# Performance work log

Measured on AMD Instinct MI355X. Metric: run time of the kernel, lower is better.

## Reference

```python
import jax, jax.numpy as jnp
import numpy as np

S, H, P, NL, PL = 128, 1024, 1024, 2, 32  # string_size, hidden, program_size, layers, program_length
T_IN, T_OUT = 64, 64


def _run_lstm(xs, h0, c0, layers):
    """Multi-layer LSTM over sequence xs [T, in]. PyTorch gate order i,f,g,o.
    h0, c0: [NL, H]. Returns (top-layer outputs [T, H], hT [NL,H], cT [NL,H])."""
    hs, cs = [], []
    for l, (Wih, Whh, bih, bhh) in enumerate(layers):
        b = bih + bhh
        def step(carry, x, Wih=Wih, Whh=Whh, b=b):
            h, c = carry
            g = Wih @ x + Whh @ h + b           # [4H]
            i, f, gg, o = jnp.split(g, 4)
            c = jax.nn.sigmoid(f) * c + jax.nn.sigmoid(i) * jnp.tanh(gg)
            h = jax.nn.sigmoid(o) * jnp.tanh(c)
            return (h, c), h
        (hT, cT), xs = jax.lax.scan(step, (h0[l], c0[l]), xs)
        hs.append(hT); cs.append(cT)
    return xs, jnp.stack(hs), jnp.stack(cs)


def setup_inputs() -> dict:
    key = jax.random.key(0)
    keys = iter(jax.random.split(key, 64))
    bound = 1.0 / np.sqrt(H)
    def u(shape):
        return jax.random.uniform(next(keys), shape, minval=-bound, maxval=bound, dtype=jnp.float32)
    d = {}
    for pre, in0 in (("in", S), ("out", S), ("pr", H)):
        for l in range(NL):
            isz = in0 if l == 0 else H
            d[f"{pre}_Wih{l}"] = u((4 * H, isz))
            d[f"{pre}_Whh{l}"] = u((4 * H, H))
            d[f"{pre}_bih{l}"] = u((4 * H,))
            d[f"{pre}_bhh{l}"] = u((4 * H,))
    d["lin_W"] = u((P, H))
    d["lin_b"] = u((P,))
    d["input_seq"] = jax.random.randint(next(keys), (T_IN,), 0, S)
    d["output_seq"] = jax.random.randint(next(keys), (T_OUT,), 0, S)
    return d


def reference(in_Wih0, in_Whh0, in_bih0, in_bhh0, in_Wih1, in_Whh1, in_bih1, in_bhh1,
              out_Wih0, out_Whh0, out_bih0, out_bhh0, out_Wih1, out_Whh1, out_bih1, out_bhh1,
              pr_Wih0, pr_Whh0, pr_bih0, pr_bhh0, pr_Wih1, pr_Whh1, pr_bih1, pr_bhh1,
              lin_W, lin_b, input_seq, output_seq):
    in_layers = [(in_Wih0, in_Whh0, in_bih0, in_bhh0), (in_Wih1, in_Whh1, in_bih1, in_bhh1)]
    out_layers = [(out_Wih0, out_Whh0, out_bih0, out_bhh0), (out_Wih1, out_Whh1, out_bih1, out_bhh1)]
    pr_layers = [(pr_Wih0, pr_Whh0, pr_bih0, pr_bhh0), (pr_Wih1, pr_Whh1, pr_bih1, pr_bhh1)]

    x_in = jax.nn.one_hot(input_seq, S, dtype=jnp.float32)    # [T_IN, S]
    x_out = jax.nn.one_hot(output_seq, S, dtype=jnp.float32)  # [T_OUT, S]

    h = jnp.zeros((NL, H), dtype=jnp.float32)
    c = jnp.zeros((NL, H), dtype=jnp.float32)
    _, h, c = _run_lstm(x_in, h, c, in_layers)
    _, h, c = _run_lstm(x_out, h, c, out_layers)

    # Faithful to source: previous_hidden is set once and never updated inside the loop,
    # so the program LSTM sees the SAME input vector at every decode step.
    prev_h = h[-1]                                            # [H]
    xs = jnp.broadcast_to(prev_h, (PL, H))
    ys, h, c = _run_lstm(xs, h, c, pr_layers)                 # [PL, H]
    return ys @ lin_W.T + lin_b                                # [PL, P]
```

## Files before the change

kernel.cpp:

```cpp
#include <hip/hip_runtime.h>
#include <hip/hip_fp16.h>
#include <cmath>

#define HDIM 1024
#define TPB 512
#define NWG 256
#define M4 4194304ull
#define WS_WOFF 65536ull
#define CVT_TOTAL 42991616ull
#define WS_NEEDED (WS_WOFF + CVT_TOTAL * 2ull)

typedef unsigned long long ulong64;
typedef unsigned int uint32;
typedef _Float16 h2f __attribute__((ext_vector_type(2)));

__device__ __forceinline__ ulong64 ld_g8(const ulong64* p) {
  return __hip_atomic_load(p, __ATOMIC_RELAXED, __HIP_MEMORY_SCOPE_AGENT);
}
__device__ __forceinline__ void st_gu(uint32* p, uint32 v) {
  __hip_atomic_store(p, v, __ATOMIC_RELAXED, __HIP_MEMORY_SCOPE_AGENT);
}

__device__ __forceinline__ float sigm(float x) { return 1.f / (1.f + __expf(-x)); }
__device__ __forceinline__ float tanh_f(float x) {
  float e = __expf(2.f * x);
  return 1.f - 2.f / (e + 1.f);
}

__device__ __forceinline__ float f4dot(float4 wf, float4 xf, float acc) {
  union { float4 f; h2f h[4]; } w, x;
  w.f = wf; x.f = xf;
#pragma unroll
  for (int i = 0; i < 4; ++i) {
#if __has_builtin(__builtin_amdgcn_fdot2)
    acc = __builtin_amdgcn_fdot2(w.h[i], x.h[i], acc, false);
#else
    acc = fmaf((float)w.h[i].x, (float)x.h[i].x, acc);
    acc = fmaf((float)w.h[i].y, (float)x.h[i].y, acc);
#endif
  }
  return acc;
}

__global__ void __launch_bounds__(TPB, 2) rf16_kernel(
    const float* __restrict__ in_Wih0, const float* __restrict__ in_bih0, const float* __restrict__ in_bhh0,
    const float* __restrict__ in_bih1, const float* __restrict__ in_bhh1,
    const float* __restrict__ out_Wih0, const float* __restrict__ out_bih0, const float* __restrict__ out_bhh0,
    const float* __restrict__ out_bih1, const float* __restrict__ out_bhh1,
    const float* __restrict__ pr_bih0, const float* __restrict__ pr_bhh0,
    const float* __restrict__ pr_bih1, const float* __restrict__ pr_bhh1,
    const float* __restrict__ lin_b,
    const int* __restrict__ in_seq, const int* __restrict__ out_seq,
    float* __restrict__ out, float* __restrict__ ws)
{
  const int tid = threadIdx.x, wg = blockIdx.x;
  const int wv = tid >> 6, lane = tid & 63;
  const int grp = lane >> 4, gl = lane & 15;
  const int cell = (wg << 2) + (wv & 3);
  const bool isL1 = wv < 4;
  const int rowi = (grp << 10) + cell;

  const __half* wb = (const __half*)((const char*)ws + WS_WOFF);
  uint32* h0T = (uint32*)((char*)ws + 4096);
  uint32* h1T = (uint32*)((char*)ws + 4096 + 16384);

  __shared__ __align__(16) ulong64 xaP[2][128], xbP[2][128];

  float c_reg = 0.f, pre0v = 0.f;
  float bA, bB, bC, lbias = 0.f;
  if (isL1) {
    bA = in_bih1[rowi] + in_bhh1[rowi];
    bB = out_bih1[rowi] + out_bhh1[rowi];
    bC = pr_bih1[rowi] + pr_bhh1[rowi];
  } else {
    bA = in_bih0[rowi] + in_bhh0[rowi];
    bB = out_bih0[rowi] + out_bhh0[rowi];
    bC = pr_bih0[rowi] + pr_bhh0[rowi];
    lbias = lin_b[cell];
  }

  int fail = 0;
  float4 wreg[16];
  float4 lw0, lw1;

  auto preload8 = [&](const __half* wrow, int base) {
    const float4* w4 = (const float4*)wrow;
#pragma unroll
    for (int j = 0; j < 8; ++j) wreg[base + j] = w4[j * 16 + gl];
  };
  auto dotx = [&](int base, const ulong64* xp, float acc) {
    const __half* x = (const __half*)xp;
#pragma unroll
    for (int j = 0; j < 8; ++j)
      acc = f4dot(wreg[base + j], *(const float4*)(x + (j * 16 + gl) * 8), acc);
    return acc;
  };
  auto red16 = [&](float v) {
#pragma unroll
    for (int o = 1; o < 16; o <<= 1) v += __shfl_xor(v, o, 64);
    return v;
  };
  auto wred64 = [&](float v) {
#pragma unroll
    for (int o = 1; o < 64; o <<= 1) v += __shfl_xor(v, o, 64);
    return v;
  };
  auto poll_pack = [&](const uint32* T, int tag, ulong64* dst) {
    if (fail) return;
    const ulong64* src = (const ulong64*)(T + ((tag & 3) << 10)) + (lane << 3);
    ulong64 d[8];
    int spins = 0;
    for (;;) {
      bool ok = true;
#pragma unroll
      for (int i = 0; i < 8; ++i) {
        d[i] = ld_g8(src + i);
        ok &= (((int)((d[i] >> 16) & 0xFFFF)) == tag) & (((int)(d[i] >> 48)) == tag);
      }
      if (__all(ok)) break;
      if (++spins > (1 << 18)) { fail = 1; return; }
      __builtin_amdgcn_s_sleep(1);
    }
    uint32 q[8];
#pragma unroll
    for (int i = 0; i < 8; ++i)
      q[i] = (uint32)(d[i] & 0xFFFF) | ((uint32)((d[i] >> 32) & 0xFFFF) << 16);
    ((uint4*)dst)[2 * lane]     = make_uint4(q[0], q[1], q[2], q[3]);
    ((uint4*)dst)[2 * lane + 1] = make_uint4(q[4], q[5], q[6], q[7]);
  };
  auto zero_pack = [&](ulong64* dst) {
    ((uint4*)dst)[2 * lane]     = make_uint4(0, 0, 0, 0);
    ((uint4*)dst)[2 * lane + 1] = make_uint4(0, 0, 0, 0);
  };
  auto produce = [&](float v, uint32* T, int tag) {
    float gi = __shfl(v, 0, 64), gf = __shfl(v, 16, 64);
    float gc = __shfl(v, 32, 64), go = __shfl(v, 48, 64);
    float c2 = sigm(gf) * c_reg + sigm(gi) * tanh_f(gc);
    c_reg = c2;
    if (lane == 0) {
      uint32 w = ((uint32)tag << 16) | (uint32)__half_as_ushort(__float2half(sigm(go) * tanh_f(c2)));
      st_gu(T + ((tag & 3) << 10) + cell, w);
    }
  };

  if (!isL1) {
    int idx = in_seq[0];
    float v = bA + in_Wih0[(size_t)rowi * 128 + idx];
    produce(v, h0T, 1);
  }

  if (isL1) {
    preload8(wb + 0 * M4 + (size_t)rowi * 1024, 0);
    preload8(wb + 1 * M4 + (size_t)rowi * 1024, 8);
  } else {
    preload8(wb + 2 * M4 + (size_t)rowi * 1024, 0);
  }

#pragma unroll 1
  for (int s = 2; s <= 128; ++s) {
    if (s == 65 && !isL1) preload8(wb + 5 * M4 + (size_t)rowi * 1024, 0);
    if (s == 66 && isL1) {
      preload8(wb + 3 * M4 + (size_t)rowi * 1024, 0);
      preload8(wb + 4 * M4 + (size_t)rowi * 1024, 8);
    }
    float wcol = 0.f;
    if (!isL1) {
      int idx = (s < 65) ? in_seq[s - 1] : out_seq[s - 65];
      wcol = ((s < 65) ? in_Wih0 : out_Wih0)[(size_t)rowi * 128 + idx];
    }
    if (wv == 0) poll_pack(h0T, s - 1, xaP[s & 1]);
    if (wv == 1) {
      if (s == 2) zero_pack(xbP[0]);
      else poll_pack(h1T, s - 1, xbP[s & 1]);
    }
    __syncthreads();
    if (isL1) {
      float v = dotx(0, xaP[s & 1], 0.f);
      v = dotx(8, xbP[s & 1], v);
      v = red16(v) + ((s < 66) ? bA : bB);
      produce(v, h1T, s);
    } else {
      float v = red16(dotx(0, xaP[s & 1], 0.f)) + ((s < 65) ? bA : bB) + wcol;
      produce(v, h0T, s);
    }
  }

  if (wv == 0) poll_pack(h0T, 128, xaP[1]);
  if (wv == 1) poll_pack(h1T, 128, xbP[1]);
  __syncthreads();
  if (isL1) {
    float v = dotx(0, xaP[1], 0.f);
    v = dotx(8, xbP[1], v);
    v = red16(v) + bB;
    produce(v, h1T, 129);
  }

  if (!isL1) {
    preload8(wb + 9 * M4 + (size_t)rowi * 1024, 0);
    preload8(wb + 8 * M4 + (size_t)rowi * 1024, 8);
  }
  if (wv == 0) poll_pack(h0T, 128, xaP[0]);
  if (wv == 1) poll_pack(h1T, 129, xbP[0]);
  __syncthreads();
  if (!isL1) {
    pre0v = red16(dotx(0, xbP[0], 0.f)) + bC;
    float v = red16(dotx(8, xaP[0], 0.f)) + pre0v;
    produce(v, h0T, 130);
  }

  if (isL1) {
    preload8(wb + 6 * M4 + (size_t)rowi * 1024, 0);
    preload8(wb + 7 * M4 + (size_t)rowi * 1024, 8);
  } else {
#pragma unroll
    for (int j = 0; j < 8; ++j) wreg[j] = wreg[8 + j];
    const float4* lwp = (const float4*)(wb + 10 * M4 + (size_t)cell * 1024);
    lw0 = lwp[lane * 2]; lw1 = lwp[lane * 2 + 1];
  }

#pragma unroll 1
  for (int s = 131; s <= 162; ++s) {
    const int tb = (s == 131) ? 129 : s - 1;
    if (wv == 0) poll_pack(h0T, s - 1, xaP[s & 1]);
    if (wv == 1) poll_pack(h1T, tb, xbP[s & 1]);
    __syncthreads();
    if (isL1) {
      float v = dotx(0, xaP[s & 1], 0.f);
      v = dotx(8, xbP[s & 1], v);
      v = red16(v) + bC;
      produce(v, h1T, s);
    } else {
      if (s >= 132) {
        const __half* x = (const __half*)xbP[s & 1];
        float a = f4dot(lw0, *(const float4*)(x + lane * 16), 0.f);
        a = f4dot(lw1, *(const float4*)(x + lane * 16 + 8), a);
        float r = wred64(a) + lbias;
        if (lane == 0) out[(size_t)(s - 132) * 1024 + cell] = r;
      }
      if (s <= 161) {
        float v = red16(dotx(0, xaP[s & 1], 0.f)) + pre0v;
        produce(v, h0T, s);
      }
    }
  }

  if (wv == 1) poll_pack(h1T, 162, xbP[1]);
  __syncthreads();
  if (!isL1) {
    const __half* x = (const __half*)xbP[1];
    float a = f4dot(lw0, *(const float4*)(x + lane * 16), 0.f);
    a = f4dot(lw1, *(const float4*)(x + lane * 16 + 8), a);
    float r = wred64(a) + lbias;
    if (lane == 0) out[(size_t)31 * 1024 + cell] = r;
  }
}

struct CvtArgs { const float* s[11]; };

__global__ void __launch_bounds__(256) cvt_kernel(CvtArgs a, __half* dst) {
  size_t i = ((size_t)blockIdx.x * 256 + threadIdx.x) * 8;
  if (i >= CVT_TOTAL) return;
  const float* sp;
  if (i < 10 * M4) sp = a.s[i >> 22] + (i & (M4 - 1));
  else sp = a.s[10] + (i - 10 * M4);
  float4 f0 = ((const float4*)sp)[0];
  float4 f1 = ((const float4*)sp)[1];
  __half2 o[4];
  o[0] = __float22half2_rn(make_float2(f0.x, f0.y));
  o[1] = __float22half2_rn(make_float2(f0.z, f0.w));
  o[2] = __float22half2_rn(make_float2(f1.x, f1.y));
  o[3] = __float22half2_rn(make_float2(f1.z, f1.w));
  *((float4*)(dst + i)) = *(float4*)o;
}

extern "C" void kernel_launch(void* const* d_in, const int* in_sizes, int n_in,
                              void* d_out, int out_size, void* d_ws, size_t ws_size,
                              hipStream_t stream) {
  (void)in_sizes; (void)n_in; (void)out_size;
  if (ws_size < WS_NEEDED) return;
  hipMemsetAsync(d_ws, 0, 40960, stream);
  const float* F[26];
  for (int i = 0; i < 26; ++i) F[i] = (const float*)d_in[i];
  const int* iseq = (const int*)d_in[26];
  const int* oseq = (const int*)d_in[27];

  CvtArgs ca;
  ca.s[0] = F[4];  ca.s[1] = F[5];  ca.s[2] = F[1];
  ca.s[3] = F[12]; ca.s[4] = F[13]; ca.s[5] = F[9];
  ca.s[6] = F[20]; ca.s[7] = F[21]; ca.s[8] = F[17];
  ca.s[9] = F[16]; ca.s[10] = F[24];
  __half* wdst = (__half*)((char*)d_ws + WS_WOFF);
  cvt_kernel<<<dim3((unsigned)(CVT_TOTAL / 8 / 256)), dim3(256), 0, stream>>>(ca, wdst);
  rf16_kernel<<<dim3(NWG), dim3(TPB), 0, stream>>>(
      F[0], F[2], F[3], F[6], F[7],
      F[8], F[10], F[11], F[14], F[15],
      F[18], F[19], F[22], F[23],
      F[25], iseq, oseq, (float*)d_out, (float*)d_ws);
}
```

Before: 787.0 us.

## Replace per-WG global polling with hierarchical checker workgroups and replicated flags

Instead of every workgroup spinning on the full 1024-entry hidden-state buffer, eight checker workgroups each poll a 64-entry slice and publish a per-slot flag into eight replicated flag arrays. All workgroups then poll only their replica's eight flag words before doing a single read of the hidden vector. This is meant to cut cross-device polling traffic and contention on the shared state lines at each of the ~160 sequential steps. The cost is an extra flag hop of latency per step and more memset and workspace setup.

```diff
diff --git a/kernel.cpp b/kernel.cpp
--- a/kernel.cpp
+++ b/kernel.cpp
@@ -6,7 +6,7 @@
 #define TPB 512
 #define NWG 256
 #define M4 4194304ull
-#define WS_WOFF 65536ull
+#define WS_WOFF 327680ull
 #define CVT_TOTAL 42991616ull
 #define WS_NEEDED (WS_WOFF + CVT_TOTAL * 2ull)
 
@@ -18,6 +18,9 @@
   return __hip_atomic_load(p, __ATOMIC_RELAXED, __HIP_MEMORY_SCOPE_AGENT);
 }
 __device__ __forceinline__ void st_gu(uint32* p, uint32 v) {
+  __hip_atomic_store(p, v, __ATOMIC_RELAXED, __HIP_MEMORY_SCOPE_AGENT);
+}
+__device__ __forceinline__ void st_gi(int* p, int v) {
   __hip_atomic_store(p, v, __ATOMIC_RELAXED, __HIP_MEMORY_SCOPE_AGENT);
 }
 
@@ -59,10 +62,13 @@
   const int cell = (wg << 2) + (wv & 3);
   const bool isL1 = wv < 4;
   const int rowi = (grp << 10) + cell;
+  const bool chkWG = (wg < 8);
 
   const __half* wb = (const __half*)((const char*)ws + WS_WOFF);
-  uint32* h0T = (uint32*)((char*)ws + 4096);
-  uint32* h1T = (uint32*)((char*)ws + 4096 + 16384);
+  uint32* h0M = (uint32*)((char*)ws + 4096);
+  uint32* h1M = (uint32*)((char*)ws + 20480);
+  int* FL = (int*)((char*)ws + 36864);
+  int* myFlag = FL + ((wg & 7) << 8);
 
   __shared__ __align__(16) ulong64 xaP[2][128], xbP[2][128];
 
@@ -105,32 +111,67 @@
     for (int o = 1; o < 64; o <<= 1) v += __shfl_xor(v, o, 64);
     return v;
   };
-  auto poll_pack = [&](const uint32* T, int tag, ulong64* dst) {
+  auto tags_ok = [&](const ulong64* d, int tag) {
+    bool ok = true;
+#pragma unroll
+    for (int i = 0; i < 8; ++i)
+      ok &= (((int)((d[i] >> 16) & 0xFFFF)) == tag) & (((int)(d[i] >> 48)) == tag);
+    return ok;
+  };
+  auto pack_lds = [&](const ulong64* d, ulong64* dst) {
+    uint32 q[8];
+#pragma unroll
+    for (int i = 0; i < 8; ++i)
+      q[i] = (uint32)(d[i] & 0xFFFF) | ((uint32)((d[i] >> 32) & 0xFFFF) << 16);
+    dst[4 * lane]     = (ulong64)q[0] | ((ulong64)q[1] << 32);
+    dst[4 * lane + 1] = (ulong64)q[2] | ((ulong64)q[3] << 32);
+    dst[4 * lane + 2] = (ulong64)q[4] | ((ulong64)q[5] << 32);
+    dst[4 * lane + 3] = (ulong64)q[6] | ((ulong64)q[7] << 32);
+  };
+  auto fetch_pack = [&](const uint32* T, int stream, int tag, ulong64* dst) {
     if (fail) return;
-    const ulong64* src = (const ulong64*)(T + ((tag & 3) << 10)) + (lane << 3);
+    const int slot = tag & 3;
+    if (chkWG) {
+      const ulong64* sl = (const ulong64*)(T + (slot << 10)) + (wg << 6) + lane;
+      int spins = 0;
+      for (;;) {
+        ulong64 w = ld_g8(sl);
+        bool ok = (((int)((w >> 16) & 0xFFFF)) == tag) & (((int)(w >> 48)) == tag);
+        if (__all(ok)) break;
+        if (++spins > (1 << 20)) { fail = 1; break; }
+      }
+      if (!fail && lane < 8)
+        st_gi(FL + (lane << 8) + (stream << 7) + (slot << 4) + wg, tag);
+    }
+    {
+      const ulong64* fp = (const ulong64*)(myFlag + (stream << 7) + (slot << 4));
+      int spins = 0;
+      for (;;) {
+        ulong64 f0 = ld_g8(fp), f1 = ld_g8(fp + 1);
+        ulong64 f2 = ld_g8(fp + 2), f3 = ld_g8(fp + 3);
+        bool ok = (((int)f0) == tag) & (((int)(f0 >> 32)) == tag) &
+                  (((int)f1) == tag) & (((int)(f1 >> 32)) == tag) &
+                  (((int)f2) == tag) & (((int)(f2 >> 32)) == tag) &
+                  (((int)f3) == tag) & (((int)(f3 >> 32)) == tag);
+        if (ok) break;
+        if (++spins > (1 << 20)) { fail = 1; return; }
+        __builtin_amdgcn_s_sleep(1);
+      }
+    }
+    const ulong64* src = (const ulong64*)(T + (slot << 10)) + (lane << 3);
     ulong64 d[8];
     int spins = 0;
     for (;;) {
-      bool ok = true;
-#pragma unroll
-      for (int i = 0; i < 8; ++i) {
-        d[i] = ld_g8(src + i);
-        ok &= (((int)((d[i] >> 16) & 0xFFFF)) == tag) & (((int)(d[i] >> 48)) == tag);
-      }
-      if (__all(ok)) break;
-      if (++spins > (1 << 18)) { fail = 1; return; }
-      __builtin_amdgcn_s_sleep(1);
-    }
-    uint32 q[8];
-#pragma unroll
-    for (int i = 0; i < 8; ++i)
-      q[i] = (uint32)(d[i] & 0xFFFF) | ((uint32)((d[i] >> 32) & 0xFFFF) << 16);
-    ((uint4*)dst)[2 * lane]     = make_uint4(q[0], q[1], q[2], q[3]);
-    ((uint4*)dst)[2 * lane + 1] = make_uint4(q[4], q[5], q[6], q[7]);
+#pragma unroll
+      for (int i = 0; i < 8; ++i) d[i] = ld_g8(src + i);
+      if (__all(tags_ok(d, tag))) break;
+      if (++spins > (1 << 16)) { fail = 1; return; }
+    }
+    pack_lds(d, dst);
   };
   auto zero_pack = [&](ulong64* dst) {
-    ((uint4*)dst)[2 * lane]     = make_uint4(0, 0, 0, 0);
-    ((uint4*)dst)[2 * lane + 1] = make_uint4(0, 0, 0, 0);
+#pragma unroll
+    for (int i = 0; i < 4; ++i) dst[4 * lane + i] = 0ull;
   };
   auto produce = [&](float v, uint32* T, int tag) {
     float gi = __shfl(v, 0, 64), gf = __shfl(v, 16, 64);
@@ -146,7 +187,7 @@
   if (!isL1) {
     int idx = in_seq[0];
     float v = bA + in_Wih0[(size_t)rowi * 128 + idx];
-    produce(v, h0T, 1);
+    produce(v, h0M, 1);
   }
 
   if (isL1) {
@@ -168,44 +209,44 @@
       int idx = (s < 65) ? in_seq[s - 1] : out_seq[s - 65];
       wcol = ((s < 65) ? in_Wih0 : out_Wih0)[(size_t)rowi * 128 + idx];
     }
-    if (wv == 0) poll_pack(h0T, s - 1, xaP[s & 1]);
+    if (wv == 0) fetch_pack(h0M, 0, s - 1, xaP[s & 1]);
     if (wv == 1) {
       if (s == 2) zero_pack(xbP[0]);
-      else poll_pack(h1T, s - 1, xbP[s & 1]);
+      else fetch_pack(h1M, 1, s - 1, xbP[s & 1]);
     }
     __syncthreads();
     if (isL1) {
       float v = dotx(0, xaP[s & 1], 0.f);
       v = dotx(8, xbP[s & 1], v);
       v = red16(v) + ((s < 66) ? bA : bB);
-      produce(v, h1T, s);
+      produce(v, h1M, s);
     } else {
       float v = red16(dotx(0, xaP[s & 1], 0.f)) + ((s < 65) ? bA : bB) + wcol;
-      produce(v, h0T, s);
-    }
-  }
-
-  if (wv == 0) poll_pack(h0T, 128, xaP[1]);
-  if (wv == 1) poll_pack(h1T, 128, xbP[1]);
+      produce(v, h0M, s);
+    }
+  }
+
+  if (wv == 0) fetch_pack(h0M, 0, 128, xaP[1]);
+  if (wv == 1) fetch_pack(h1M, 1, 128, xbP[1]);
   __syncthreads();
   if (isL1) {
     float v = dotx(0, xaP[1], 0.f);
     v = dotx(8, xbP[1], v);
     v = red16(v) + bB;
-    produce(v, h1T, 129);
+    produce(v, h1M, 129);
   }
 
   if (!isL1) {
     preload8(wb + 9 * M4 + (size_t)rowi * 1024, 0);
     preload8(wb + 8 * M4 + (size_t)rowi * 1024, 8);
   }
-  if (wv == 0) poll_pack(h0T, 128, xaP[0]);
-  if (wv == 1) poll_pack(h1T, 129, xbP[0]);
+  if (wv == 0) fetch_pack(h0M, 0, 128, xaP[0]);
+  if (wv == 1) fetch_pack(h1M, 1, 129, xbP[0]);
   __syncthreads();
   if (!isL1) {
     pre0v = red16(dotx(0, xbP[0], 0.f)) + bC;
     float v = red16(dotx(8, xaP[0], 0.f)) + pre0v;
-    produce(v, h0T, 130);
+    produce(v, h0M, 130);
   }
 
   if (isL1) {
@@ -221,14 +262,14 @@
 #pragma unroll 1
   for (int s = 131; s <= 162; ++s) {
     const int tb = (s == 131) ? 129 : s - 1;
-    if (wv == 0) poll_pack(h0T, s - 1, xaP[s & 1]);
-    if (wv == 1) poll_pack(h1T, tb, xbP[s & 1]);
+    if (wv == 0) fetch_pack(h0M, 0, s - 1, xaP[s & 1]);
+    if (wv == 1) fetch_pack(h1M, 1, tb, xbP[s & 1]);
     __syncthreads();
     if (isL1) {
       float v = dotx(0, xaP[s & 1], 0.f);
       v = dotx(8, xbP[s & 1], v);
       v = red16(v) + bC;
-      produce(v, h1T, s);
+      produce(v, h1M, s);
     } else {
       if (s >= 132) {
         const __half* x = (const __half*)xbP[s & 1];
@@ -239,12 +280,12 @@
       }
       if (s <= 161) {
         float v = red16(dotx(0, xaP[s & 1], 0.f)) + pre0v;
-        produce(v, h0T, s);
+        produce(v, h0M, s);
       }
     }
   }
 
-  if (wv == 1) poll_pack(h1T, 162, xbP[1]);
+  if (wv == 1) fetch_pack(h1M, 1, 162, xbP[1]);
   __syncthreads();
   if (!isL1) {
     const __half* x = (const __half*)xbP[1];
@@ -278,7 +319,7 @@
                               hipStream_t stream) {
   (void)in_sizes; (void)n_in; (void)out_size;
   if (ws_size < WS_NEEDED) return;
-  hipMemsetAsync(d_ws, 0, 40960, stream);
+  (void)hipMemsetAsync(d_ws, 0, 45056, stream);
   const float* F[26];
   for (int i = 0; i < 26; ++i) F[i] = (const float*)d_in[i];
   const int* iseq = (const int*)d_in[26];
```

Result: faster. 654.6 us, median of 2 (-16.8%).

## Replicate hidden-state exchange buffers into 8 mirrors to spread polling traffic

Applied to the files above, without the earlier changes.

Each producer now writes its tagged fp16 hidden value into 8 mirror copies of the exchange buffer instead of one. Consumer workgroups poll only the mirror selected by their workgroup index modulo 8, so the 256 workgroups spin on different memory lines rather than one shared set. This is meant to cut contention and cache-line ping-pong in the cross-workgroup step barrier, at the cost of eight times as many stores per step and a larger workspace memset. The LDS pack is also rewritten to use 64-bit stores instead of uint4 stores.

```diff
diff --git a/kernel.cpp b/kernel.cpp
--- a/kernel.cpp
+++ b/kernel.cpp
@@ -6,7 +6,7 @@
 #define TPB 512
 #define NWG 256
 #define M4 4194304ull
-#define WS_WOFF 65536ull
+#define WS_WOFF 327680ull
 #define CVT_TOTAL 42991616ull
 #define WS_NEEDED (WS_WOFF + CVT_TOTAL * 2ull)
 
@@ -61,8 +61,9 @@
   const int rowi = (grp << 10) + cell;
 
   const __half* wb = (const __half*)((const char*)ws + WS_WOFF);
-  uint32* h0T = (uint32*)((char*)ws + 4096);
-  uint32* h1T = (uint32*)((char*)ws + 4096 + 16384);
+  uint32* h0Mir = (uint32*)((char*)ws + 4096);
+  uint32* h1Mir = (uint32*)((char*)ws + 4096 + 131072);
+  const int myMir = (wg & 7) << 12;
 
   __shared__ __align__(16) ulong64 xaP[2][128], xbP[2][128];
 
@@ -105,48 +106,55 @@
     for (int o = 1; o < 64; o <<= 1) v += __shfl_xor(v, o, 64);
     return v;
   };
-  auto poll_pack = [&](const uint32* T, int tag, ulong64* dst) {
+  auto tags_ok = [&](const ulong64* d, int tag) {
+    bool ok = true;
+#pragma unroll
+    for (int i = 0; i < 8; ++i)
+      ok &= (((int)((d[i] >> 16) & 0xFFFF)) == tag) & (((int)(d[i] >> 48)) == tag);
+    return ok;
+  };
+  auto pack_lds = [&](const ulong64* d, ulong64* dst) {
+    uint32 q[8];
+#pragma unroll
+    for (int i = 0; i < 8; ++i)
+      q[i] = (uint32)(d[i] & 0xFFFF) | ((uint32)((d[i] >> 32) & 0xFFFF) << 16);
+    dst[4 * lane]     = (ulong64)q[0] | ((ulong64)q[1] << 32);
+    dst[4 * lane + 1] = (ulong64)q[2] | ((ulong64)q[3] << 32);
+    dst[4 * lane + 2] = (ulong64)q[4] | ((ulong64)q[5] << 32);
+    dst[4 * lane + 3] = (ulong64)q[6] | ((ulong64)q[7] << 32);
+  };
+  auto fetch_pack = [&](const uint32* Mir, int tag, ulong64* dst) {
     if (fail) return;
-    const ulong64* src = (const ulong64*)(T + ((tag & 3) << 10)) + (lane << 3);
+    const ulong64* src = (const ulong64*)(Mir + myMir + ((tag & 3) << 10)) + (lane << 3);
     ulong64 d[8];
     int spins = 0;
     for (;;) {
-      bool ok = true;
-#pragma unroll
-      for (int i = 0; i < 8; ++i) {
-        d[i] = ld_g8(src + i);
-        ok &= (((int)((d[i] >> 16) & 0xFFFF)) == tag) & (((int)(d[i] >> 48)) == tag);
-      }
-      if (__all(ok)) break;
+#pragma unroll
+      for (int i = 0; i < 8; ++i) d[i] = ld_g8(src + i);
+      if (__all(tags_ok(d, tag))) break;
       if (++spins > (1 << 18)) { fail = 1; return; }
       __builtin_amdgcn_s_sleep(1);
     }
-    uint32 q[8];
-#pragma unroll
-    for (int i = 0; i < 8; ++i)
-      q[i] = (uint32)(d[i] & 0xFFFF) | ((uint32)((d[i] >> 32) & 0xFFFF) << 16);
-    ((uint4*)dst)[2 * lane]     = make_uint4(q[0], q[1], q[2], q[3]);
-    ((uint4*)dst)[2 * lane + 1] = make_uint4(q[4], q[5], q[6], q[7]);
+    pack_lds(d, dst);
   };
   auto zero_pack = [&](ulong64* dst) {
-    ((uint4*)dst)[2 * lane]     = make_uint4(0, 0, 0, 0);
-    ((uint4*)dst)[2 * lane + 1] = make_uint4(0, 0, 0, 0);
-  };
-  auto produce = [&](float v, uint32* T, int tag) {
+#pragma unroll
+    for (int i = 0; i < 4; ++i) dst[4 * lane + i] = 0ull;
+  };
+  auto produce = [&](float v, uint32* Mir, int tag) {
     float gi = __shfl(v, 0, 64), gf = __shfl(v, 16, 64);
     float gc = __shfl(v, 32, 64), go = __shfl(v, 48, 64);
     float c2 = sigm(gf) * c_reg + sigm(gi) * tanh_f(gc);
     c_reg = c2;
-    if (lane == 0) {
-      uint32 w = ((uint32)tag << 16) | (uint32)__half_as_ushort(__float2half(sigm(go) * tanh_f(c2)));
-      st_gu(T + ((tag & 3) << 10) + cell, w);
-    }
+    uint32 w = ((uint32)tag << 16) | (uint32)__half_as_ushort(__float2half(sigm(go) * tanh_f(c2)));
+    if (lane < 8)
+      st_gu(Mir + (lane << 12) + ((tag & 3) << 10) + cell, w);
   };
 
   if (!isL1) {
     int idx = in_seq[0];
     float v = bA + in_Wih0[(size_t)rowi * 128 + idx];
-    produce(v, h0T, 1);
+    produce(v, h0Mir, 1);
   }
 
   if (isL1) {
@@ -168,44 +176,44 @@
       int idx = (s < 65) ? in_seq[s - 1] : out_seq[s - 65];
       wcol = ((s < 65) ? in_Wih0 : out_Wih0)[(size_t)rowi * 128 + idx];
     }
-    if (wv == 0) poll_pack(h0T, s - 1, xaP[s & 1]);
+    if (wv == 0) fetch_pack(h0Mir, s - 1, xaP[s & 1]);
     if (wv == 1) {
       if (s == 2) zero_pack(xbP[0]);
-      else poll_pack(h1T, s - 1, xbP[s & 1]);
+      else fetch_pack(h1Mir, s - 1, xbP[s & 1]);
     }
     __syncthreads();
     if (isL1) {
       float v = dotx(0, xaP[s & 1], 0.f);
       v = dotx(8, xbP[s & 1], v);
       v = red16(v) + ((s < 66) ? bA : bB);
-      produce(v, h1T, s);
+      produce(v, h1Mir, s);
     } else {
       float v = red16(dotx(0, xaP[s & 1], 0.f)) + ((s < 65) ? bA : bB) + wcol;
-      produce(v, h0T, s);
-    }
-  }
-
-  if (wv == 0) poll_pack(h0T, 128, xaP[1]);
-  if (wv == 1) poll_pack(h1T, 128, xbP[1]);
+      produce(v, h0Mir, s);
+    }
+  }
+
+  if (wv == 0) fetch_pack(h0Mir, 128, xaP[1]);
+  if (wv == 1) fetch_pack(h1Mir, 128, xbP[1]);
   __syncthreads();
   if (isL1) {
     float v = dotx(0, xaP[1], 0.f);
     v = dotx(8, xbP[1], v);
     v = red16(v) + bB;
-    produce(v, h1T, 129);
+    produce(v, h1Mir, 129);
   }
 
   if (!isL1) {
     preload8(wb + 9 * M4 + (size_t)rowi * 1024, 0);
     preload8(wb + 8 * M4 + (size_t)rowi * 1024, 8);
   }
-  if (wv == 0) poll_pack(h0T, 128, xaP[0]);
-  if (wv == 1) poll_pack(h1T, 129, xbP[0]);
+  if (wv == 0) fetch_pack(h0Mir, 128, xaP[0]);
+  if (wv == 1) fetch_pack(h1Mir, 129, xbP[0]);
   __syncthreads();
   if (!isL1) {
     pre0v = red16(dotx(0, xbP[0], 0.f)) + bC;
     float v = red16(dotx(8, xaP[0], 0.f)) + pre0v;
-    produce(v, h0T, 130);
+    produce(v, h0Mir, 130);
   }
 
   if (isL1) {
@@ -221,14 +229,14 @@
 #pragma unroll 1
   for (int s = 131; s <= 162; ++s) {
     const int tb = (s == 131) ? 129 : s - 1;
-    if (wv == 0) poll_pack(h0T, s - 1, xaP[s & 1]);
-    if (wv == 1) poll_pack(h1T, tb, xbP[s & 1]);
+    if (wv == 0) fetch_pack(h0Mir, s - 1, xaP[s & 1]);
+    if (wv == 1) fetch_pack(h1Mir, tb, xbP[s & 1]);
     __syncthreads();
     if (isL1) {
       float v = dotx(0, xaP[s & 1], 0.f);
       v = dotx(8, xbP[s & 1], v);
       v = red16(v) + bC;
-      produce(v, h1T, s);
+      produce(v, h1Mir, s);
     } else {
       if (s >= 132) {
         const __half* x = (const __half*)xbP[s & 1];
@@ -239,12 +247,12 @@
       }
       if (s <= 161) {
         float v = red16(dotx(0, xaP[s & 1], 0.f)) + pre0v;
-        produce(v, h0T, s);
+        produce(v, h0Mir, s);
       }
     }
   }
 
-  if (wv == 1) poll_pack(h1T, 162, xbP[1]);
+  if (wv == 1) fetch_pack(h1Mir, 162, xbP[1]);
   __syncthreads();
   if (!isL1) {
     const __half* x = (const __half*)xbP[1];
@@ -278,7 +286,7 @@
                               hipStream_t stream) {
   (void)in_sizes; (void)n_in; (void)out_size;
   if (ws_size < WS_NEEDED) return;
-  hipMemsetAsync(d_ws, 0, 40960, stream);
+  (void)hipMemsetAsync(d_ws, 0, 266240, stream);
   const float* F[26];
   for (int i = 0; i < 26; ++i) F[i] = (const float*)d_in[i];
   const int* iseq = (const int*)d_in[26];
```

Result: faster. 729.5 us (-7.3%).
